# Kernel tuning notes

Hardware: AMD Instinct MI355X
Metric: run time of the kernel (lower is better)

The kernel has to match this reference:

```python
import jax, jax.numpy as jnp
import numpy as np

B, N, IN_DIM, HEADS, PER_HEAD = 8, 512, 256, 4, 32
OUT_DIM = HEADS * PER_HEAD  # 128
NEG_SLOPE = 0.2


def setup_inputs() -> dict:
    key = jax.random.key(0)
    ks = jax.random.split(key, 8)
    x = jax.random.normal(ks[0], (B, N, IN_DIM), jnp.float32)
    adj = jax.random.randint(ks[1], (B, N, N), 0, 2, jnp.int32)
    sl = 1.0 / np.sqrt(IN_DIM)
    W_l = jax.random.normal(ks[2], (IN_DIM, OUT_DIM), jnp.float32) * sl  # source proj
    b_l = jnp.zeros((OUT_DIM,), jnp.float32)
    W_r = jax.random.normal(ks[3], (IN_DIM, OUT_DIM), jnp.float32) * sl  # target proj
    b_r = jnp.zeros((OUT_DIM,), jnp.float32)
    att = jax.random.normal(ks[4], (HEADS, PER_HEAD), jnp.float32) * (1.0 / np.sqrt(PER_HEAD))
    bias = jnp.zeros((OUT_DIM,), jnp.float32)
    return {"x": x, "adj": adj, "W_l": W_l, "b_l": b_l, "W_r": W_r, "b_r": b_r,
            "att": att, "bias": bias}


def _gatv2_single(x_b, adj_b, W_l, b_l, W_r, b_r, att, bias):
    # PyG GATv2Conv: remove_self_loops + add_self_loops -> diagonal forced to 1
    n = x_b.shape[0]
    adj_sl = jnp.fill_diagonal(adj_b, 1, inplace=False)
    # edge_index = adj.nonzero().t(): source = row, target = col
    m = (adj_sl != 0).T  # m[i, j]: source j feeds target i
    xl = (x_b @ W_l + b_l).reshape(n, HEADS, PER_HEAD)  # source-side features
    xr = (x_b @ W_r + b_r).reshape(n, HEADS, PER_HEAD)  # target-side features
    s = xr[:, None] + xl[None, :]                       # [i, j, H, C]
    s = jnp.where(s > 0, s, NEG_SLOPE * s)              # LeakyReLU(0.2)
    e = jnp.einsum('ijhc,hc->ijh', s, att)              # attention logits
    e = jnp.where(m[..., None], e, -jnp.inf)
    alpha = jax.nn.softmax(e, axis=1)                   # softmax over sources j
    out = jnp.einsum('ijh,jhc->ihc', alpha, xl).reshape(n, HEADS * PER_HEAD)
    return out + bias


def reference(x, adj, W_l, b_l, W_r, b_r, att, bias):
    # Sequential per-batch processing, faithful to the original Python loop
    # and keeping the [N,N,H,C] intermediate to one graph at a time.
    def one(args):
        x_b, adj_b = args
        return _gatv2_single(x_b, adj_b, W_l, b_l, W_r, b_r, att, bias)
    return jax.lax.map(one, (x, adj))  # [B, N, OUT_DIM]
```

## Files before the change

kernel.cpp:

```cpp
#include <hip/hip_runtime.h>
#include <hip/hip_bf16.h>

#define B_   8
#define N_   512
#define IND  256
#define H_   4
#define PH   32
#define OD   128
#define TI   4

typedef float v2f __attribute__((ext_vector_type(2)));

#define ATT_SCALE 0.5770780163555854f
#define DLR_SCALE 0.8656170245333781f

template <int PAT>
__device__ __forceinline__ float dpp_add(float x) {
    int yi = __builtin_amdgcn_mov_dpp(__float_as_int(x), PAT, 0xF, 0xF, true);
    return x + __int_as_float(yi);
}

__device__ __forceinline__ float fast_exp2(float x) {
#if __has_builtin(__builtin_amdgcn_exp2f)
    return __builtin_amdgcn_exp2f(x);
#else
    return exp2f(x);
#endif
}

__device__ __forceinline__ void pk_fma(v2f& d, v2f a, v2f b) {
    asm("v_pk_fma_f32 %0, %1, %2, %0" : "+v"(d) : "v"(a), "v"(b));
}
__device__ __forceinline__ v2f pk_add(v2f a, v2f b) {
    v2f d;
    asm("v_pk_add_f32 %0, %1, %2" : "=v"(d) : "v"(a), "v"(b));
    return d;
}

__global__ __launch_bounds__(256) void pack_kernel(
    const int* __restrict__ adj, unsigned long long* __restrict__ pack)
{
    const int t = threadIdx.x;
    const int lane = t & 63;
    const int r = blockIdx.x * 4 + (t >> 6);
    const int j = r & (N_ - 1);
    const int* row = adj + (size_t)r * N_;
    #pragma unroll
    for (int k = 0; k < 8; ++k) {
        const int i = k * 64 + lane;
        int a = row[i];
        unsigned long long m = __ballot(a != 0 || i == j);
        if (lane == 0) pack[(size_t)r * 8 + k] = m;
    }
}

__global__ __launch_bounds__(256, 2) void proj_kernel(
    const float* __restrict__ x,
    const float* __restrict__ Wl, const float* __restrict__ bl,
    const float* __restrict__ Wr, const float* __restrict__ br,
    const float* __restrict__ att,
    float* __restrict__ xl, float* __restrict__ xr,
    float* __restrict__ dl, float* __restrict__ dr)
{
    __shared__ float xs[8 * IND];
    const int t = threadIdx.x;
    const int row0 = blockIdx.x * 8;

    const float4* xp4 = (const float4*)(x + (size_t)row0 * IND);
    float4* xs4 = (float4*)xs;
    #pragma unroll
    for (int k = 0; k < 2; ++k)
        xs4[t + k * 256] = xp4[t + k * 256];
    __syncthreads();

    const int which = t >> 7;
    const int rg = (t >> 6) & 1;
    const int og = t & 63;
    const int o0 = og * 2;
    const int r0 = rg * 4;
    const float* W  = which ? Wr : Wl;
    const float* bb = which ? br : bl;

    float acc0[4], acc1[4];
    #pragma unroll
    for (int r = 0; r < 4; ++r) { acc0[r] = 0.f; acc1[r] = 0.f; }

    for (int k = 0; k < IND; k += 4) {
        float wf0[4], wf1[4];
        #pragma unroll
        for (int kk = 0; kk < 4; ++kk) {
            float2 wv = *(const float2*)(W + (size_t)(k + kk) * OD + o0);
            wf0[kk] = wv.x;
            wf1[kk] = wv.y;
        }
        float xv[4][4];
        #pragma unroll
        for (int r = 0; r < 4; ++r)
            *(float4*)(xv[r]) = *(const float4*)(&xs[(r0 + r) * IND + k]);
        #pragma unroll
        for (int kk = 0; kk < 4; ++kk)
            #pragma unroll
            for (int r = 0; r < 4; ++r) {
                acc0[r] = fmaf(xv[r][kk], wf0[kk], acc0[r]);
                acc1[r] = fmaf(xv[r][kk], wf1[kk], acc1[r]);
            }
    }

    const float bv0 = bb[o0];
    const float bv1 = bb[o0 + 1];
    const float a0 = att[o0];
    const float a1 = att[o0 + 1];
    float* dst = which ? xr : xl;
    float* dp  = which ? dr : dl;
    float dcon[4];
    #pragma unroll
    for (int r = 0; r < 4; ++r) {
        float y0 = acc0[r] + bv0;
        float y1 = acc1[r] + bv1;
        *(float2*)(&dst[(size_t)(row0 + r0 + r) * OD + o0]) = make_float2(y0, y1);
        dcon[r] = fmaf(a0, y0, a1 * y1);
    }
    #pragma unroll
    for (int m = 1; m < 16; m <<= 1) {
        #pragma unroll
        for (int r = 0; r < 4; ++r)
            dcon[r] += __shfl_xor(dcon[r], m);
    }
    if ((og & 15) == 0) {
        const int h = og >> 4;
        #pragma unroll
        for (int r = 0; r < 4; ++r)
            dp[(size_t)(row0 + r0 + r) * H_ + h] = DLR_SCALE * dcon[r];
    }
}

__global__ __launch_bounds__(256, 3) void attn_kernel(
    const unsigned* __restrict__ pack, const float* __restrict__ att,
    const float* __restrict__ bias,
    const float* __restrict__ xl, const float* __restrict__ xr,
    const float* __restrict__ dl, const float* __restrict__ dr,
    float* __restrict__ out)
{
    const int t = threadIdx.x;
    const int b  = blockIdx.x >> 7;
    const int i0 = (blockIdx.x & 127) * TI;
    const int cq = t & 3;
    const int js = (t >> 2) & 15;
    const int h  = t >> 6;
    const int cbase = h * PH + cq * 8;
    const int shift = i0 & 31;

    float atS[8];
    {
        const float* ap = att + cbase;
        float4 a0 = *(const float4*)(ap);
        float4 a1 = *(const float4*)(ap + 4);
        atS[0] = ATT_SCALE * a0.x; atS[1] = ATT_SCALE * a0.y;
        atS[2] = ATT_SCALE * a0.z; atS[3] = ATT_SCALE * a0.w;
        atS[4] = ATT_SCALE * a1.x; atS[5] = ATT_SCALE * a1.y;
        atS[6] = ATT_SCALE * a1.z; atS[7] = ATT_SCALE * a1.w;
    }
    v2f xr2[TI][4];
    float drv[TI];
    #pragma unroll
    for (int il = 0; il < TI; ++il) {
        const float* xp = xr + ((size_t)(b * N_ + i0 + il)) * OD + cbase;
        float4 r0 = *(const float4*)(xp);
        float4 r1 = *(const float4*)(xp + 4);
        xr2[il][0] = (v2f){r0.x, r0.y};
        xr2[il][1] = (v2f){r0.z, r0.w};
        xr2[il][2] = (v2f){r1.x, r1.y};
        xr2[il][3] = (v2f){r1.z, r1.w};
        drv[il] = dr[((size_t)(b * N_ + i0 + il)) * H_ + h];
    }

    v2f acc[TI][4];
    float sumw[TI];
    #pragma unroll
    for (int il = 0; il < TI; ++il) {
        sumw[il] = 0.f;
        #pragma unroll
        for (int m = 0; m < 4; ++m) acc[il][m] = (v2f){0.f, 0.f};
    }

    const float*    xlp = xl + ((size_t)(b * N_ + js)) * OD + cbase;
    const unsigned* pp  = pack + ((size_t)(b * N_ + js)) * 16 + (i0 >> 5);
    const float*    dlp = dl + ((size_t)(b * N_ + js)) * H_ + h;

    float4   va = *(const float4*)(xlp);
    float4   vb = *(const float4*)(xlp + 4);
    unsigned pj = *pp;
    float    dj = *dlp;

    #pragma unroll 2
    for (int u = 0; u < 32; ++u) {
        float4   wa = va, wb = vb;
        unsigned wp = pj;
        float    wd = dj;
        if (u < 31) {
            xlp += 16 * OD; pp += 16 * 16; dlp += 16 * H_;
            va = *(const float4*)(xlp);
            vb = *(const float4*)(xlp + 4);
            pj = *pp;
            dj = *dlp;
        }
        const unsigned pbs = wp >> shift;
        v2f p0 = (v2f){wa.x, wa.y}, p1 = (v2f){wa.z, wa.w};
        v2f p2 = (v2f){wb.x, wb.y}, p3 = (v2f){wb.z, wb.w};
        #pragma unroll
        for (int il = 0; il < TI; ++il) {
            float e2a = 0.f, e2b = 0.f;
            v2f s;
            s = pk_add(xr2[il][0], p0);
            e2a = fmaf(atS[0], __builtin_fabsf(s.x), e2a);
            e2b = fmaf(atS[1], __builtin_fabsf(s.y), e2b);
            s = pk_add(xr2[il][1], p1);
            e2a = fmaf(atS[2], __builtin_fabsf(s.x), e2a);
            e2b = fmaf(atS[3], __builtin_fabsf(s.y), e2b);
            s = pk_add(xr2[il][2], p2);
            e2a = fmaf(atS[4], __builtin_fabsf(s.x), e2a);
            e2b = fmaf(atS[5], __builtin_fabsf(s.y), e2b);
            s = pk_add(xr2[il][3], p3);
            e2a = fmaf(atS[6], __builtin_fabsf(s.x), e2a);
            e2b = fmaf(atS[7], __builtin_fabsf(s.y), e2b);
            float eh = e2a + e2b;
            eh = dpp_add<0xB1>(eh);
            eh = dpp_add<0x4E>(eh);
            float e = (wd + drv[il]) + eh;
            float ex = fast_exp2(e);
            float w = (pbs & (1u << il)) ? ex : 0.f;
            sumw[il] += w;
            v2f ws = (v2f){w, w};
            pk_fma(acc[il][0], ws, p0);
            pk_fma(acc[il][1], ws, p1);
            pk_fma(acc[il][2], ws, p2);
            pk_fma(acc[il][3], ws, p3);
        }
    }

    #pragma unroll
    for (int il = 0; il < TI; ++il) {
        sumw[il] += __shfl_xor(sumw[il], 4);
        sumw[il] += __shfl_xor(sumw[il], 8);
        sumw[il] += __shfl_xor(sumw[il], 16);
        sumw[il] += __shfl_xor(sumw[il], 32);
    }

    float accf[32];
    #pragma unroll
    for (int il = 0; il < TI; ++il)
        #pragma unroll
        for (int m = 0; m < 4; ++m) {
            accf[il * 8 + 2 * m]     = acc[il][m].x;
            accf[il * 8 + 2 * m + 1] = acc[il][m].y;
        }

    float r16[16];
    {
        const bool hi = (js & 1) != 0;
        #pragma unroll
        for (int m = 0; m < 16; ++m) {
            float send = hi ? accf[m] : accf[16 + m];
            float keep = hi ? accf[16 + m] : accf[m];
            r16[m] = keep + __shfl_xor(send, 4);
        }
    }
    float r8[8];
    {
        const bool hi = (js & 2) != 0;
        #pragma unroll
        for (int m = 0; m < 8; ++m) {
            float send = hi ? r16[m] : r16[8 + m];
            float keep = hi ? r16[8 + m] : r16[m];
            r8[m] = keep + __shfl_xor(send, 8);
        }
    }
    float r4[4];
    {
        const bool hi = (js & 4) != 0;
        #pragma unroll
        for (int m = 0; m < 4; ++m) {
            float send = hi ? r8[m] : r8[4 + m];
            float keep = hi ? r8[4 + m] : r8[m];
            r4[m] = keep + __shfl_xor(send, 16);
        }
    }
    float r2[2];
    {
        const bool hi = (js & 8) != 0;
        #pragma unroll
        for (int m = 0; m < 2; ++m) {
            float send = hi ? r4[m] : r4[2 + m];
            float keep = hi ? r4[2 + m] : r4[m];
            r2[m] = keep + __shfl_xor(send, 32);
        }
    }

    const int il = ((js & 1) << 1) | ((js >> 1) & 1);
    const int coff = ((js >> 2) & 1) * 4 + ((js >> 3) & 1) * 2;
    const int c = cbase + coff;
    const float sw0 = (js & 1) ? ((js & 2) ? sumw[3] : sumw[2])
                               : ((js & 2) ? sumw[1] : sumw[0]);
    const float inv = 1.f / sw0;
    float* op = out + ((size_t)(b * N_ + i0 + il)) * OD;
    *(float2*)(&op[c]) = make_float2(fmaf(r2[0], inv, bias[c]),
                                     fmaf(r2[1], inv, bias[c + 1]));
}

extern "C" void kernel_launch(void* const* d_in, const int* in_sizes, int n_in,
                              void* d_out, int out_size, void* d_ws, size_t ws_size,
                              hipStream_t stream) {
    const float* x    = (const float*)d_in[0];
    const int*   adj  = (const int*)d_in[1];
    const float* Wl   = (const float*)d_in[2];
    const float* bl   = (const float*)d_in[3];
    const float* Wr   = (const float*)d_in[4];
    const float* br   = (const float*)d_in[5];
    const float* att  = (const float*)d_in[6];
    const float* bias = (const float*)d_in[7];
    float* out = (float*)d_out;

    float* xl = (float*)d_ws;
    float* xr = xl + (size_t)B_ * N_ * OD;
    float* dl = xr + (size_t)B_ * N_ * OD;
    float* dr = dl + (size_t)B_ * N_ * H_;
    unsigned long long* pack =
        (unsigned long long*)(dr + (size_t)B_ * N_ * H_);

    pack_kernel<<<1024, 256, 0, stream>>>(adj, pack);
    proj_kernel<<<512, 256, 0, stream>>>(x, Wl, bl, Wr, br, att, xl, xr, dl, dr);
    attn_kernel<<<1024, 256, 0, stream>>>((const unsigned*)pack, att, bias,
                                          xl, xr, dl, dr, out);
}
```

Measured before the change: 126.0 us.

## Split attention over source halves with combine kernel and transposed mask layouts

The attention kernel now splits the 512 sources into two halves, doubling the grid to 2048 blocks. Each block writes unnormalized partial accumulators and partial softmax sums to workspace, and a new combine kernel adds the halves, normalizes and applies bias. The adjacency bitmask is repacked into a transposed per-4-target nibble byte layout, and the dl/dr logits are transposed so per-source loads are contiguous. This trades an extra kernel launch and partial-result round trips through memory for more parallelism and cheaper mask and logit loads.

```diff
diff --git a/kernel.cpp b/kernel.cpp
--- a/kernel.cpp
+++ b/kernel.cpp
@@ -38,19 +38,24 @@
 }
 
 __global__ __launch_bounds__(256) void pack_kernel(
-    const int* __restrict__ adj, unsigned long long* __restrict__ pack)
+    const int* __restrict__ adj, unsigned char* __restrict__ packT)
 {
     const int t = threadIdx.x;
     const int lane = t & 63;
     const int r = blockIdx.x * 4 + (t >> 6);
     const int j = r & (N_ - 1);
+    const int b = r >> 9;
     const int* row = adj + (size_t)r * N_;
     #pragma unroll
     for (int k = 0; k < 8; ++k) {
         const int i = k * 64 + lane;
         int a = row[i];
         unsigned long long m = __ballot(a != 0 || i == j);
-        if (lane == 0) pack[(size_t)r * 8 + k] = m;
+        if (lane < 16) {
+            const int iq = k * 16 + lane;
+            packT[((size_t)(b * 128 + iq)) * N_ + j] =
+                (unsigned char)((m >> (lane * 4)) & 15ull);
+        }
     }
 }
 
@@ -60,7 +65,7 @@
     const float* __restrict__ Wr, const float* __restrict__ br,
     const float* __restrict__ att,
     float* __restrict__ xl, float* __restrict__ xr,
-    float* __restrict__ dl, float* __restrict__ dr)
+    float* __restrict__ dlT, float* __restrict__ drT)
 {
     __shared__ float xs[8 * IND];
     const int t = threadIdx.x;
@@ -111,7 +116,7 @@
     const float a0 = att[o0];
     const float a1 = att[o0 + 1];
     float* dst = which ? xr : xl;
-    float* dp  = which ? dr : dl;
+    float* dp  = which ? drT : dlT;
     float dcon[4];
     #pragma unroll
     for (int r = 0; r < 4; ++r) {
@@ -129,26 +134,31 @@
     if ((og & 15) == 0) {
         const int h = og >> 4;
         #pragma unroll
-        for (int r = 0; r < 4; ++r)
-            dp[(size_t)(row0 + r0 + r) * H_ + h] = DLR_SCALE * dcon[r];
+        for (int r = 0; r < 4; ++r) {
+            const int n = row0 + r0 + r;
+            const int bb2 = n >> 9, nn = n & (N_ - 1);
+            dp[((size_t)(bb2 * H_ + h)) * N_ + nn] = DLR_SCALE * dcon[r];
+        }
     }
 }
 
 __global__ __launch_bounds__(256, 3) void attn_kernel(
-    const unsigned* __restrict__ pack, const float* __restrict__ att,
-    const float* __restrict__ bias,
+    const unsigned char* __restrict__ packT,
+    const float* __restrict__ att,
     const float* __restrict__ xl, const float* __restrict__ xr,
-    const float* __restrict__ dl, const float* __restrict__ dr,
-    float* __restrict__ out)
+    const float* __restrict__ dlT, const float* __restrict__ drT,
+    float* __restrict__ pacc, float* __restrict__ psum)
 {
     const int t = threadIdx.x;
-    const int b  = blockIdx.x >> 7;
-    const int i0 = (blockIdx.x & 127) * TI;
+    const int s   = blockIdx.x & 1;
+    const int blk = blockIdx.x >> 1;
+    const int b  = blk >> 7;
+    const int i0 = (blk & 127) * TI;
     const int cq = t & 3;
     const int js = (t >> 2) & 15;
     const int h  = t >> 6;
     const int cbase = h * PH + cq * 8;
-    const int shift = i0 & 31;
+    const int j0 = s * 256;
 
     float atS[8];
     {
@@ -171,7 +181,7 @@
         xr2[il][1] = (v2f){r0.z, r0.w};
         xr2[il][2] = (v2f){r1.x, r1.y};
         xr2[il][3] = (v2f){r1.z, r1.w};
-        drv[il] = dr[((size_t)(b * N_ + i0 + il)) * H_ + h];
+        drv[il] = drT[((size_t)(b * H_ + h)) * N_ + i0 + il];
     }
 
     v2f acc[TI][4];
@@ -183,52 +193,51 @@
         for (int m = 0; m < 4; ++m) acc[il][m] = (v2f){0.f, 0.f};
     }
 
-    const float*    xlp = xl + ((size_t)(b * N_ + js)) * OD + cbase;
-    const unsigned* pp  = pack + ((size_t)(b * N_ + js)) * 16 + (i0 >> 5);
-    const float*    dlp = dl + ((size_t)(b * N_ + js)) * H_ + h;
+    const float*         xlp = xl + ((size_t)(b * N_ + j0 + js)) * OD + cbase;
+    const unsigned char* ptp = packT + ((size_t)(b * 128 + (i0 >> 2))) * N_ + j0 + js;
+    const float*         dlp = dlT + ((size_t)(b * H_ + h)) * N_ + j0 + js;
 
     float4   va = *(const float4*)(xlp);
     float4   vb = *(const float4*)(xlp + 4);
-    unsigned pj = *pp;
+    unsigned pj = *ptp;
     float    dj = *dlp;
 
     #pragma unroll 2
-    for (int u = 0; u < 32; ++u) {
+    for (int u = 0; u < 16; ++u) {
         float4   wa = va, wb = vb;
         unsigned wp = pj;
         float    wd = dj;
-        if (u < 31) {
-            xlp += 16 * OD; pp += 16 * 16; dlp += 16 * H_;
+        if (u < 15) {
+            xlp += 16 * OD; ptp += 16; dlp += 16;
             va = *(const float4*)(xlp);
             vb = *(const float4*)(xlp + 4);
-            pj = *pp;
+            pj = *ptp;
             dj = *dlp;
         }
-        const unsigned pbs = wp >> shift;
         v2f p0 = (v2f){wa.x, wa.y}, p1 = (v2f){wa.z, wa.w};
         v2f p2 = (v2f){wb.x, wb.y}, p3 = (v2f){wb.z, wb.w};
         #pragma unroll
         for (int il = 0; il < TI; ++il) {
             float e2a = 0.f, e2b = 0.f;
-            v2f s;
-            s = pk_add(xr2[il][0], p0);
-            e2a = fmaf(atS[0], __builtin_fabsf(s.x), e2a);
-            e2b = fmaf(atS[1], __builtin_fabsf(s.y), e2b);
-            s = pk_add(xr2[il][1], p1);
-            e2a = fmaf(atS[2], __builtin_fabsf(s.x), e2a);
-            e2b = fmaf(atS[3], __builtin_fabsf(s.y), e2b);
-            s = pk_add(xr2[il][2], p2);
-            e2a = fmaf(atS[4], __builtin_fabsf(s.x), e2a);
-            e2b = fmaf(atS[5], __builtin_fabsf(s.y), e2b);
-            s = pk_add(xr2[il][3], p3);
-            e2a = fmaf(atS[6], __builtin_fabsf(s.x), e2a);
-            e2b = fmaf(atS[7], __builtin_fabsf(s.y), e2b);
+            v2f sv;
+            sv = pk_add(xr2[il][0], p0);
+            e2a = fmaf(atS[0], __builtin_fabsf(sv.x), e2a);
+            e2b = fmaf(atS[1], __builtin_fabsf(sv.y), e2b);
+            sv = pk_add(xr2[il][1], p1);
+            e2a = fmaf(atS[2], __builtin_fabsf(sv.x), e2a);
+            e2b = fmaf(atS[3], __builtin_fabsf(sv.y), e2b);
+            sv = pk_add(xr2[il][2], p2);
+            e2a = fmaf(atS[4], __builtin_fabsf(sv.x), e2a);
+            e2b = fmaf(atS[5], __builtin_fabsf(sv.y), e2b);
+            sv = pk_add(xr2[il][3], p3);
+            e2a = fmaf(atS[6], __builtin_fabsf(sv.x), e2a);
+            e2b = fmaf(atS[7], __builtin_fabsf(sv.y), e2b);
             float eh = e2a + e2b;
             eh = dpp_add<0xB1>(eh);
             eh = dpp_add<0x4E>(eh);
             float e = (wd + drv[il]) + eh;
             float ex = fast_exp2(e);
-            float w = (pbs & (1u << il)) ? ex : 0.f;
+            float w = (wp & (1u << il)) ? ex : 0.f;
             sumw[il] += w;
             v2f ws = (v2f){w, w};
             pk_fma(acc[il][0], ws, p0);
@@ -299,12 +308,32 @@
     const int il = ((js & 1) << 1) | ((js >> 1) & 1);
     const int coff = ((js >> 2) & 1) * 4 + ((js >> 3) & 1) * 2;
     const int c = cbase + coff;
-    const float sw0 = (js & 1) ? ((js & 2) ? sumw[3] : sumw[2])
-                               : ((js & 2) ? sumw[1] : sumw[0]);
-    const float inv = 1.f / sw0;
-    float* op = out + ((size_t)(b * N_ + i0 + il)) * OD;
-    *(float2*)(&op[c]) = make_float2(fmaf(r2[0], inv, bias[c]),
-                                     fmaf(r2[1], inv, bias[c + 1]));
+    float* pa = pacc + (size_t)s * (B_ * N_ * OD)
+                     + ((size_t)(b * N_ + i0 + il)) * OD + c;
+    *(float2*)pa = make_float2(r2[0], r2[1]);
+    if ((t & 63) == 0) {
+        float* ps = psum + s * (B_ * N_ * H_);
+        #pragma unroll
+        for (int q = 0; q < TI; ++q)
+            ps[(size_t)(b * N_ + i0 + q) * H_ + h] = sumw[q];
+    }
+}
+
+__global__ __launch_bounds__(256) void combine_kernel(
+    const float* __restrict__ pacc, const float* __restrict__ psum,
+    const float* __restrict__ bias, float* __restrict__ out)
+{
+    const int idx = blockIdx.x * 256 + threadIdx.x;
+    const int n = idx >> 6;
+    const int c = (idx & 63) * 2;
+    const int h = c >> 5;
+    float2 a0 = *(const float2*)(pacc + (size_t)n * OD + c);
+    float2 a1 = *(const float2*)(pacc + (size_t)B_ * N_ * OD + (size_t)n * OD + c);
+    float sden = psum[(size_t)n * H_ + h] + psum[B_ * N_ * H_ + (size_t)n * H_ + h];
+    float inv = 1.f / sden;
+    *(float2*)(out + (size_t)n * OD + c) =
+        make_float2(fmaf(a0.x + a1.x, inv, bias[c]),
+                    fmaf(a0.y + a1.y, inv, bias[c + 1]));
 }
 
 extern "C" void kernel_launch(void* const* d_in, const int* in_sizes, int n_in,
@@ -320,15 +349,18 @@
     const float* bias = (const float*)d_in[7];
     float* out = (float*)d_out;
 
-    float* xl = (float*)d_ws;
-    float* xr = xl + (size_t)B_ * N_ * OD;
-    float* dl = xr + (size_t)B_ * N_ * OD;
-    float* dr = dl + (size_t)B_ * N_ * H_;
-    unsigned long long* pack =
-        (unsigned long long*)(dr + (size_t)B_ * N_ * H_);
-
-    pack_kernel<<<1024, 256, 0, stream>>>(adj, pack);
-    proj_kernel<<<512, 256, 0, stream>>>(x, Wl, bl, Wr, br, att, xl, xr, dl, dr);
-    attn_kernel<<<1024, 256, 0, stream>>>((const unsigned*)pack, att, bias,
-                                          xl, xr, dl, dr, out);
-}
+    float* ws = (float*)d_ws;
+    float* xl   = ws;
+    float* xr   = xl + (size_t)B_ * N_ * OD;
+    float* dlT  = xr + (size_t)B_ * N_ * OD;
+    float* drT  = dlT + (size_t)B_ * N_ * H_;
+    float* pacc = drT + (size_t)B_ * N_ * H_;
+    float* psum = pacc + (size_t)2 * B_ * N_ * OD;
+    unsigned char* packT =
+        (unsigned char*)(psum + (size_t)2 * B_ * N_ * H_);
+
+    pack_kernel<<<1024, 256, 0, stream>>>(adj, packT);
+    proj_kernel<<<512, 256, 0, stream>>>(x, Wl, bl, Wr, br, att, xl, xr, dlT, drT);
+    attn_kernel<<<2048, 256, 0, stream>>>(packT, att, xl, xr, dlT, drT, pacc, psum);
+    combine_kernel<<<1024, 256, 0, stream>>>(pacc, psum, bias, out);
+}
```

Result: slower. 132.2 us (+4.9%).
